# Optimization experiments

Measured on AMD Instinct MI355X. Metric: run time of the kernel, lower is better.

## Reference

```python
import jax, jax.numpy as jnp
import numpy as np

INPUT_SIZE = 4
HIDDEN = 100
OUTPUT = 1
SEQ_LEN = 65536


def setup_inputs() -> dict:
    key = jax.random.key(0)
    ks = jax.random.split(key, 7)
    s = 0.1  # small init scale, mimics torch's uniform(-1/sqrt(H), 1/sqrt(H))
    return {
        "input_seq": jax.random.normal(ks[0], (SEQ_LEN, INPUT_SIZE), dtype=jnp.float32),
        "W_ih": jax.random.normal(ks[1], (4 * HIDDEN, INPUT_SIZE), dtype=jnp.float32) * s,
        "W_hh": jax.random.normal(ks[2], (4 * HIDDEN, HIDDEN), dtype=jnp.float32) * s,
        "b_ih": jax.random.normal(ks[3], (4 * HIDDEN,), dtype=jnp.float32) * s,
        "b_hh": jax.random.normal(ks[4], (4 * HIDDEN,), dtype=jnp.float32) * s,
        "W_lin": jax.random.normal(ks[5], (OUTPUT, HIDDEN), dtype=jnp.float32) * s,
        "b_lin": jax.random.normal(ks[6], (OUTPUT,), dtype=jnp.float32) * s,
    }


def reference(input_seq, W_ih, W_hh, b_ih, b_hh, W_lin, b_lin):
    # Precompute the input contribution to all gates in one GEMM: [S, 4H]
    x_gates = input_seq @ W_ih.T + (b_ih + b_hh)

    def step(carry, xg):
        h, c = carry  # each [H]
        gates = xg + h @ W_hh.T  # [4H]
        # torch gate order: i, f, g, o
        i = jax.nn.sigmoid(gates[:HIDDEN])
        f = jax.nn.sigmoid(gates[HIDDEN:2 * HIDDEN])
        g = jnp.tanh(gates[2 * HIDDEN:3 * HIDDEN])
        o = jax.nn.sigmoid(gates[3 * HIDDEN:])
        c_new = f * c + i * g
        h_new = o * jnp.tanh(c_new)
        return (h_new, c_new), None

    h0 = jnp.zeros((HIDDEN,), dtype=input_seq.dtype)
    c0 = jnp.zeros((HIDDEN,), dtype=input_seq.dtype)
    (h_last, _), _ = jax.lax.scan(step, (h0, c0), x_gates)

    # predictions[-1] == linear applied to the last hidden state; shape [OUTPUT]
    return h_last @ W_lin.T + b_lin
```

## Files before the change

### kernel.cpp

```cpp
#include <hip/hip_runtime.h>

#define HIDDEN  100
#define SEQLEN  65536
#define XTILE   256
#define NT      256

typedef float    f32x4 __attribute__((ext_vector_type(4)));
typedef _Float16 h16x2 __attribute__((ext_vector_type(2)));

#define DPP_XOR1 0xB1
#define DPP_XOR2 0x4E

#if defined(__has_builtin) && __has_builtin(__builtin_amdgcn_rcpf)
#define RCPF(x) __builtin_amdgcn_rcpf(x)
#else
#define RCPF(x) (1.0f / (x))
#endif

#define QSWAP(v, ctrl) __int_as_float(__builtin_amdgcn_mov_dpp(__float_as_int(v), (ctrl), 0xf, 0xf, true))

static __device__ __forceinline__ h16x2 as_h2(unsigned u) {
    union { unsigned u; h16x2 h; } cv; cv.u = u; return cv.h;
}
static __device__ __forceinline__ unsigned pack_f16(float a, float b) {
#if defined(__has_builtin) && __has_builtin(__builtin_amdgcn_cvt_pkrtz)
    auto v = __builtin_amdgcn_cvt_pkrtz(a, b);
    union { decltype(v) h; unsigned u; } cv; cv.h = v;
    return cv.u;
#else
    union { h16x2 h; unsigned u; } cv;
    cv.h.x = (_Float16)a; cv.h.y = (_Float16)b;
    return cv.u;
#endif
}
static __device__ __forceinline__ float dot2(h16x2 a, h16x2 b, float c) {
#if defined(__has_builtin) && __has_builtin(__builtin_amdgcn_fdot2)
    return __builtin_amdgcn_fdot2(a, b, c, false);
#else
    return __builtin_fmaf((float)a.y, (float)b.y, __builtin_fmaf((float)a.x, (float)b.x, c));
#endif
}

__global__ __launch_bounds__(NT) __attribute__((amdgpu_waves_per_eu(1, 1)))
void lstm_seq7(const float* __restrict__ x,
               const float* __restrict__ W_ih,
               const float* __restrict__ W_hh,
               const float* __restrict__ b_ih,
               const float* __restrict__ b_hh,
               const float* __restrict__ W_lin,
               const float* __restrict__ b_lin,
               float* __restrict__ out)
{
    __shared__ __align__(16) unsigned hbuf[2][64];
    __shared__ __align__(16) f32x4 xs[XTILE];
    __shared__ float red[112];

    const int tid = threadIdx.x;
    const int j   = tid >> 1;
    const int p   = tid & 1;
    const bool active = (j < HIDDEN);
    const int jj  = active ? j : 0;
    const int off = p * 50;

    h16x2 w[4][28];
    float wx0[4], wx1[4], bz[4];
#pragma unroll
    for (int g = 0; g < 4; ++g) {
        const int row = g * HIDDEN + jj;
        const float* wr = W_hh + row * HIDDEN + off;
#pragma unroll
        for (int q = 0; q < 25; ++q) {
            h16x2 pw; pw.x = (_Float16)wr[2*q]; pw.y = (_Float16)wr[2*q+1];
            w[g][q] = pw;
        }
#pragma unroll
        for (int q = 25; q < 28; ++q) w[g][q] = (h16x2)(_Float16)0;
        const f32x4 wih = reinterpret_cast<const f32x4*>(W_ih)[row];
        wx0[g] = p ? wih.z : wih.x;
        wx1[g] = p ? wih.w : wih.y;
        bz[g]  = p ? 0.f : (b_ih[row] + b_hh[row]);
    }
    float c = 0.f;

    if (tid < 64) { hbuf[0][tid] = 0u; hbuf[1][tid] = 0u; }
    __syncthreads();

    auto step = [&](const unsigned* hr, unsigned* hw, const f32x4 xv) {
        const uint4* h4 = reinterpret_cast<const uint4*>(hr + (p ? 28 : 0));
        uint4 hv[7];
#pragma unroll
        for (int t = 0; t < 7; ++t) hv[t] = h4[t];

        const float xe0 = p ? xv.z : xv.x;
        const float xe1 = p ? xv.w : xv.y;
        float a0 = __builtin_fmaf(wx1[0], xe1, __builtin_fmaf(wx0[0], xe0, bz[0]));
        float a1 = __builtin_fmaf(wx1[1], xe1, __builtin_fmaf(wx0[1], xe0, bz[1]));
        float a2 = __builtin_fmaf(wx1[2], xe1, __builtin_fmaf(wx0[2], xe0, bz[2]));
        float a3 = __builtin_fmaf(wx1[3], xe1, __builtin_fmaf(wx0[3], xe0, bz[3]));
#pragma unroll
        for (int t = 0; t < 7; ++t) {
            const h16x2 h0 = as_h2(hv[t].x), h1 = as_h2(hv[t].y);
            const h16x2 h2 = as_h2(hv[t].z), h3 = as_h2(hv[t].w);
            a0 = dot2(w[0][4*t+0], h0, a0); a1 = dot2(w[1][4*t+0], h0, a1);
            a2 = dot2(w[2][4*t+0], h0, a2); a3 = dot2(w[3][4*t+0], h0, a3);
            a0 = dot2(w[0][4*t+1], h1, a0); a1 = dot2(w[1][4*t+1], h1, a1);
            a2 = dot2(w[2][4*t+1], h1, a2); a3 = dot2(w[3][4*t+1], h1, a3);
            a0 = dot2(w[0][4*t+2], h2, a0); a1 = dot2(w[1][4*t+2], h2, a1);
            a2 = dot2(w[2][4*t+2], h2, a2); a3 = dot2(w[3][4*t+2], h2, a3);
            a0 = dot2(w[0][4*t+3], h3, a0); a1 = dot2(w[1][4*t+3], h3, a1);
            a2 = dot2(w[2][4*t+3], h3, a2); a3 = dot2(w[3][4*t+3], h3, a3);
        }
        a0 += QSWAP(a0, DPP_XOR1);
        a1 += QSWAP(a1, DPP_XOR1);
        a2 += QSWAP(a2, DPP_XOR1);
        a3 += QSWAP(a3, DPP_XOR1);

        const float i_ = RCPF(1.0f + __expf(-a0));
        const float f_ = RCPF(1.0f + __expf(-a1));
        const float g_ = __builtin_fmaf(-2.0f, RCPF(1.0f + __expf(2.0f * a2)), 1.0f);
        const float o_ = RCPF(1.0f + __expf(-a3));
        c = __builtin_fmaf(f_, c, i_ * g_);
        const float th   = __builtin_fmaf(-2.0f, RCPF(1.0f + __expf(2.0f * c)), 1.0f);
        const float hval = o_ * th;

        const float hoth = QSWAP(hval, DPP_XOR2);
        if ((tid & 3) == 0 && active) {
            const int m  = tid >> 2;
            const int dw = (m < 25) ? m : m + 3;
            hw[dw] = pack_f16(hval, hoth);
        }
        __syncthreads();
    };

    const f32x4* x4 = reinterpret_cast<const f32x4*>(x);
    for (int t0 = 0; t0 < SEQLEN; t0 += XTILE) {
        xs[tid] = x4[t0 + tid];
        __syncthreads();
        for (int tt = 0; tt < XTILE; tt += 2) {
            step(hbuf[0], hbuf[1], xs[tt]);
            step(hbuf[1], hbuf[0], xs[tt + 1]);
        }
    }

    if (tid < HIDDEN) {
        const int slot = (tid < 50) ? tid : tid + 6;
        const h16x2 hp = as_h2(hbuf[0][slot >> 1]);
        const float hj = (slot & 1) ? (float)hp.y : (float)hp.x;
        red[tid] = hj * W_lin[tid];
    }
    __syncthreads();
    if (tid == 0) {
        float s = b_lin[0];
        for (int q = 0; q < HIDDEN; ++q) s += red[q];
        out[0] = s;
    }
}

extern "C" void kernel_launch(void* const* d_in, const int* in_sizes, int n_in,
                              void* d_out, int out_size, void* d_ws, size_t ws_size,
                              hipStream_t stream) {
    const float* x     = (const float*)d_in[0];
    const float* W_ih  = (const float*)d_in[1];
    const float* W_hh  = (const float*)d_in[2];
    const float* b_ih  = (const float*)d_in[3];
    const float* b_hh  = (const float*)d_in[4];
    const float* W_lin = (const float*)d_in[5];
    const float* b_lin = (const float*)d_in[6];
    float* out = (float*)d_out;

    lstm_seq7<<<dim3(1), dim3(NT), 0, stream>>>(
        x, W_ih, W_hh, b_ih, b_hh, W_lin, b_lin, out);
}
```

Measured before the change: 26.69 ms.

## Split each hidden unit across four lanes and spread gate activations across lanes

Doubles the block to 512 threads so each hidden unit's recurrent dot product is split across four lanes of 25 inputs each instead of two lanes of 50. Partial sums are combined with two DPP steps, and each lane computes one gate activation with a unified sigmoid/tanh formula; the four gate values are then broadcast with DPP quad permutes. The aim is to shorten the serial per-step critical path of dot2 chains and transcendentals. The cost is eight waves to synchronize at every timestep barrier instead of four, plus narrower half-precision stores to LDS.

Result: slower. 29.32 ms (+9.8%).

```diff
diff --git a/kernel.cpp b/kernel.cpp
--- a/kernel.cpp
+++ b/kernel.cpp
@@ -3,13 +3,17 @@
 #define HIDDEN  100
 #define SEQLEN  65536
 #define XTILE   256
-#define NT      256
+#define NT      512
 
-typedef float    f32x4 __attribute__((ext_vector_type(4)));
+typedef float    f32x2v __attribute__((ext_vector_type(2)));
 typedef _Float16 h16x2 __attribute__((ext_vector_type(2)));
 
 #define DPP_XOR1 0xB1
 #define DPP_XOR2 0x4E
+#define DPP_BC0  0x00
+#define DPP_BC1  0x55
+#define DPP_BC2  0xAA
+#define DPP_BC3  0xFF
 
 #if defined(__has_builtin) && __has_builtin(__builtin_amdgcn_rcpf)
 #define RCPF(x) __builtin_amdgcn_rcpf(x)
@@ -17,21 +21,10 @@
 #define RCPF(x) (1.0f / (x))
 #endif
 
-#define QSWAP(v, ctrl) __int_as_float(__builtin_amdgcn_mov_dpp(__float_as_int(v), (ctrl), 0xf, 0xf, true))
+#define QP(v, ctrl) __int_as_float(__builtin_amdgcn_mov_dpp(__float_as_int(v), (ctrl), 0xf, 0xf, true))
 
 static __device__ __forceinline__ h16x2 as_h2(unsigned u) {
     union { unsigned u; h16x2 h; } cv; cv.u = u; return cv.h;
-}
-static __device__ __forceinline__ unsigned pack_f16(float a, float b) {
-#if defined(__has_builtin) && __has_builtin(__builtin_amdgcn_cvt_pkrtz)
-    auto v = __builtin_amdgcn_cvt_pkrtz(a, b);
-    union { decltype(v) h; unsigned u; } cv; cv.h = v;
-    return cv.u;
-#else
-    union { h16x2 h; unsigned u; } cv;
-    cv.h.x = (_Float16)a; cv.h.y = (_Float16)b;
-    return cv.u;
-#endif
 }
 static __device__ __forceinline__ float dot2(h16x2 a, h16x2 b, float c) {
 #if defined(__has_builtin) && __has_builtin(__builtin_amdgcn_fdot2)
@@ -41,8 +34,8 @@
 #endif
 }
 
-__global__ __launch_bounds__(NT) __attribute__((amdgpu_waves_per_eu(1, 1)))
-void lstm_seq7(const float* __restrict__ x,
+__global__ __launch_bounds__(NT) __attribute__((amdgpu_waves_per_eu(2, 2)))
+void lstm_seq9(const float* __restrict__ x,
                const float* __restrict__ W_ih,
                const float* __restrict__ W_hh,
                const float* __restrict__ b_ih,
@@ -52,101 +45,127 @@
                float* __restrict__ out)
 {
     __shared__ __align__(16) unsigned hbuf[2][64];
-    __shared__ __align__(16) f32x4 xs[XTILE];
-    __shared__ float red[112];
+    __shared__ __align__(16) float    xsf[XTILE * 4];
+    __shared__ float red[128];
 
     const int tid = threadIdx.x;
-    const int j   = tid >> 1;
-    const int p   = tid & 1;
+    const int j   = tid >> 2;
+    const int r   = tid & 3;
     const bool active = (j < HIDDEN);
     const int jj  = active ? j : 0;
-    const int off = p * 50;
+    const int off = r * 25;
 
-    h16x2 w[4][28];
-    float wx0[4], wx1[4], bz[4];
+    h16x2 w[4][13];
+    float wx[4], bz[4];
 #pragma unroll
     for (int g = 0; g < 4; ++g) {
         const int row = g * HIDDEN + jj;
         const float* wr = W_hh + row * HIDDEN + off;
 #pragma unroll
-        for (int q = 0; q < 25; ++q) {
+        for (int q = 0; q < 12; ++q) {
             h16x2 pw; pw.x = (_Float16)wr[2*q]; pw.y = (_Float16)wr[2*q+1];
             w[g][q] = pw;
         }
-#pragma unroll
-        for (int q = 25; q < 28; ++q) w[g][q] = (h16x2)(_Float16)0;
-        const f32x4 wih = reinterpret_cast<const f32x4*>(W_ih)[row];
-        wx0[g] = p ? wih.z : wih.x;
-        wx1[g] = p ? wih.w : wih.y;
-        bz[g]  = p ? 0.f : (b_ih[row] + b_hh[row]);
+        { h16x2 pw; pw.x = (_Float16)wr[24]; pw.y = (_Float16)0; w[g][12] = pw; }
+        wx[g] = W_ih[row * 4 + r];
+        bz[g] = (r == 0) ? (b_ih[row] + b_hh[row]) : 0.f;
     }
+    const float mm  = (r == 2) ? 2.0f : 1.0f;
+    const float mm1 = mm - 1.0f;
     float c = 0.f;
 
-    if (tid < 64) { hbuf[0][tid] = 0u; hbuf[1][tid] = 0u; }
+    if (tid < 128) ((unsigned*)hbuf)[tid] = 0u;
     __syncthreads();
 
-    auto step = [&](const unsigned* hr, unsigned* hw, const f32x4 xv) {
-        const uint4* h4 = reinterpret_cast<const uint4*>(hr + (p ? 28 : 0));
-        uint4 hv[7];
-#pragma unroll
-        for (int t = 0; t < 7; ++t) hv[t] = h4[t];
+    const int wslot = 32 * (jj / 25) + (jj % 25);
 
-        const float xe0 = p ? xv.z : xv.x;
-        const float xe1 = p ? xv.w : xv.y;
-        float a0 = __builtin_fmaf(wx1[0], xe1, __builtin_fmaf(wx0[0], xe0, bz[0]));
-        float a1 = __builtin_fmaf(wx1[1], xe1, __builtin_fmaf(wx0[1], xe0, bz[1]));
-        float a2 = __builtin_fmaf(wx1[2], xe1, __builtin_fmaf(wx0[2], xe0, bz[2]));
-        float a3 = __builtin_fmaf(wx1[3], xe1, __builtin_fmaf(wx0[3], xe0, bz[3]));
-#pragma unroll
-        for (int t = 0; t < 7; ++t) {
-            const h16x2 h0 = as_h2(hv[t].x), h1 = as_h2(hv[t].y);
-            const h16x2 h2 = as_h2(hv[t].z), h3 = as_h2(hv[t].w);
-            a0 = dot2(w[0][4*t+0], h0, a0); a1 = dot2(w[1][4*t+0], h0, a1);
-            a2 = dot2(w[2][4*t+0], h0, a2); a3 = dot2(w[3][4*t+0], h0, a3);
-            a0 = dot2(w[0][4*t+1], h1, a0); a1 = dot2(w[1][4*t+1], h1, a1);
-            a2 = dot2(w[2][4*t+1], h1, a2); a3 = dot2(w[3][4*t+1], h1, a3);
-            a0 = dot2(w[0][4*t+2], h2, a0); a1 = dot2(w[1][4*t+2], h2, a1);
-            a2 = dot2(w[2][4*t+2], h2, a2); a3 = dot2(w[3][4*t+2], h2, a3);
-            a0 = dot2(w[0][4*t+3], h3, a0); a1 = dot2(w[1][4*t+3], h3, a1);
-            a2 = dot2(w[2][4*t+3], h3, a2); a3 = dot2(w[3][4*t+3], h3, a3);
+    auto step = [&](int rd, int wrb, int tt) {
+        const uint4* h4 = reinterpret_cast<const uint4*>(hbuf[rd] + 16 * r);
+        const uint4 hv0 = h4[0], hv1 = h4[1], hv2 = h4[2];
+        const unsigned hv3 = hbuf[rd][16 * r + 12];
+        const float xe = xsf[tt * 4 + r];
+
+        float a0 = __builtin_fmaf(wx[0], xe, bz[0]);
+        float a1 = __builtin_fmaf(wx[1], xe, bz[1]);
+        float a2 = __builtin_fmaf(wx[2], xe, bz[2]);
+        float a3 = __builtin_fmaf(wx[3], xe, bz[3]);
+
+        {
+            const h16x2 h0 = as_h2(hv0.x), h1 = as_h2(hv0.y);
+            const h16x2 h2 = as_h2(hv0.z), h3 = as_h2(hv0.w);
+            a0 = dot2(w[0][0], h0, a0); a1 = dot2(w[1][0], h0, a1);
+            a2 = dot2(w[2][0], h0, a2); a3 = dot2(w[3][0], h0, a3);
+            a0 = dot2(w[0][1], h1, a0); a1 = dot2(w[1][1], h1, a1);
+            a2 = dot2(w[2][1], h1, a2); a3 = dot2(w[3][1], h1, a3);
+            a0 = dot2(w[0][2], h2, a0); a1 = dot2(w[1][2], h2, a1);
+            a2 = dot2(w[2][2], h2, a2); a3 = dot2(w[3][2], h2, a3);
+            a0 = dot2(w[0][3], h3, a0); a1 = dot2(w[1][3], h3, a1);
+            a2 = dot2(w[2][3], h3, a2); a3 = dot2(w[3][3], h3, a3);
         }
-        a0 += QSWAP(a0, DPP_XOR1);
-        a1 += QSWAP(a1, DPP_XOR1);
-        a2 += QSWAP(a2, DPP_XOR1);
-        a3 += QSWAP(a3, DPP_XOR1);
+        {
+            const h16x2 h0 = as_h2(hv1.x), h1 = as_h2(hv1.y);
+            const h16x2 h2 = as_h2(hv1.z), h3 = as_h2(hv1.w);
+            a0 = dot2(w[0][4], h0, a0); a1 = dot2(w[1][4], h0, a1);
+            a2 = dot2(w[2][4], h0, a2); a3 = dot2(w[3][4], h0, a3);
+            a0 = dot2(w[0][5], h1, a0); a1 = dot2(w[1][5], h1, a1);
+            a2 = dot2(w[2][5], h1, a2); a3 = dot2(w[3][5], h1, a3);
+            a0 = dot2(w[0][6], h2, a0); a1 = dot2(w[1][6], h2, a1);
+            a2 = dot2(w[2][6], h2, a2); a3 = dot2(w[3][6], h2, a3);
+            a0 = dot2(w[0][7], h3, a0); a1 = dot2(w[1][7], h3, a1);
+            a2 = dot2(w[2][7], h3, a2); a3 = dot2(w[3][7], h3, a3);
+        }
+        {
+            const h16x2 h0 = as_h2(hv2.x), h1 = as_h2(hv2.y);
+            const h16x2 h2 = as_h2(hv2.z), h3 = as_h2(hv2.w);
+            a0 = dot2(w[0][8],  h0, a0); a1 = dot2(w[1][8],  h0, a1);
+            a2 = dot2(w[2][8],  h0, a2); a3 = dot2(w[3][8],  h0, a3);
+            a0 = dot2(w[0][9],  h1, a0); a1 = dot2(w[1][9],  h1, a1);
+            a2 = dot2(w[2][9],  h1, a2); a3 = dot2(w[3][9],  h1, a3);
+            a0 = dot2(w[0][10], h2, a0); a1 = dot2(w[1][10], h2, a1);
+            a2 = dot2(w[2][10], h2, a2); a3 = dot2(w[3][10], h2, a3);
+            a0 = dot2(w[0][11], h3, a0); a1 = dot2(w[1][11], h3, a1);
+            a2 = dot2(w[2][11], h3, a2); a3 = dot2(w[3][11], h3, a3);
+        }
+        {
+            const h16x2 h12 = as_h2(hv3);
+            a0 = dot2(w[0][12], h12, a0); a1 = dot2(w[1][12], h12, a1);
+            a2 = dot2(w[2][12], h12, a2); a3 = dot2(w[3][12], h12, a3);
+        }
+        a0 += QP(a0, DPP_XOR1); a1 += QP(a1, DPP_XOR1);
+        a2 += QP(a2, DPP_XOR1); a3 += QP(a3, DPP_XOR1);
+        a0 += QP(a0, DPP_XOR2); a1 += QP(a1, DPP_XOR2);
+        a2 += QP(a2, DPP_XOR2); a3 += QP(a3, DPP_XOR2);
 
-        const float i_ = RCPF(1.0f + __expf(-a0));
-        const float f_ = RCPF(1.0f + __expf(-a1));
-        const float g_ = __builtin_fmaf(-2.0f, RCPF(1.0f + __expf(2.0f * a2)), 1.0f);
-        const float o_ = RCPF(1.0f + __expf(-a3));
+        const float s   = (r & 2) ? ((r & 1) ? a3 : a2) : ((r & 1) ? a1 : a0);
+        const float act = __builtin_fmaf(mm, RCPF(1.0f + __expf(-s * mm)), -mm1);
+
+        const float i_ = QP(act, DPP_BC0);
+        const float f_ = QP(act, DPP_BC1);
+        const float g_ = QP(act, DPP_BC2);
+        const float o_ = QP(act, DPP_BC3);
+
         c = __builtin_fmaf(f_, c, i_ * g_);
         const float th   = __builtin_fmaf(-2.0f, RCPF(1.0f + __expf(2.0f * c)), 1.0f);
         const float hval = o_ * th;
 
-        const float hoth = QSWAP(hval, DPP_XOR2);
-        if ((tid & 3) == 0 && active) {
-            const int m  = tid >> 2;
-            const int dw = (m < 25) ? m : m + 3;
-            hw[dw] = pack_f16(hval, hoth);
-        }
+        if (r == 0 && active)
+            ((_Float16*)hbuf[wrb])[wslot] = (_Float16)hval;
         __syncthreads();
     };
 
-    const f32x4* x4 = reinterpret_cast<const f32x4*>(x);
+    const f32x2v* x2 = reinterpret_cast<const f32x2v*>(x);
     for (int t0 = 0; t0 < SEQLEN; t0 += XTILE) {
-        xs[tid] = x4[t0 + tid];
+        reinterpret_cast<f32x2v*>(xsf)[tid] = x2[t0 * 2 + tid];
         __syncthreads();
         for (int tt = 0; tt < XTILE; tt += 2) {
-            step(hbuf[0], hbuf[1], xs[tt]);
-            step(hbuf[1], hbuf[0], xs[tt + 1]);
+            step(0, 1, tt);
+            step(1, 0, tt + 1);
         }
     }
 
     if (tid < HIDDEN) {
-        const int slot = (tid < 50) ? tid : tid + 6;
-        const h16x2 hp = as_h2(hbuf[0][slot >> 1]);
-        const float hj = (slot & 1) ? (float)hp.y : (float)hp.x;
-        red[tid] = hj * W_lin[tid];
+        const int slot = 32 * (tid / 25) + (tid % 25);
+        red[tid] = (float)((const _Float16*)hbuf[0])[slot] * W_lin[tid];
     }
     __syncthreads();
     if (tid == 0) {
@@ -168,6 +187,6 @@
     const float* b_lin = (const float*)d_in[6];
     float* out = (float*)d_out;
 
-    lstm_seq7<<<dim3(1), dim3(NT), 0, stream>>>(
+    lstm_seq9<<<dim3(1), dim3(NT), 0, stream>>>(
         x, W_ih, W_hh, b_ih, b_hh, W_lin, b_lin, out);
 }
```
